# Optimization experiments

Hardware: AMD Instinct MI355X
Metric: run time of the kernel (lower is better)

## Reference

```python
import jax, jax.numpy as jnp
import numpy as np

# physics constants (match init_kwargs)
DT = 1.0 / 60.0
G_ACC = 9.81
RHO = 1.225
CD = 0.47
NU = 0.001
B, N, GRID = 512, 64, 16


def _norm(x):
    return jnp.linalg.norm(x, axis=-1, keepdims=True)


def _deriv(pos, vel, rot, omega, mass, inertia, contacts, fluid_v,
           Fext, tau, log_A, log_k, log_b, conv_w):
    g_vec = jnp.array([0.0, 0.0, -G_ACC], dtype=pos.dtype)
    Fg = mass[..., None] * g_vec                                  # [B,N,3]
    A = jax.nn.softplus(log_A).reshape(1, -1, 1)
    vm = jnp.maximum(_norm(vel), 1e-6)
    Fd = -0.5 * RHO * CD * A * vm * vel                           # drag
    k = jax.nn.softplus(log_k)
    b = jax.nn.softplus(log_b)
    d_ij = pos[:, None, :, :] - pos[:, :, None, :]                # [B,N,N,3] = p_j - p_i
    dist = jnp.maximum(_norm(d_ij), 1e-6)
    n_hat = d_ij / dist
    pen = jax.nn.relu(1.0 - dist[..., 0])                         # penetration depth
    dvel = vel[:, None, :, :] - vel[:, :, None, :]                # v_j - v_i
    Fc = (k * pen[..., None] * n_hat + b * dvel * contacts[..., None]).sum(axis=2)
    dv = (Fext + Fg + Fd + Fc) / mass[..., None]
    Io = inertia * omega
    domega = (tau - jnp.cross(omega, Io)) / jnp.maximum(inertia, 1e-6)
    w, x, y, z = rot[..., 0], rot[..., 1], rot[..., 2], rot[..., 3]
    ox, oy, oz = omega[..., 0], omega[..., 1], omega[..., 2]
    drot = 0.5 * jnp.stack([
        -x * ox - y * oy - z * oz,
        w * ox + y * oz - z * oy,
        w * oy - x * oz + z * ox,
        w * oz + x * oy - y * ox], axis=-1)
    P_in = (Fext * vel).sum((-1, -2))
    P_dis = -(Fd * vel).sum((-1, -2))
    dE = P_in - P_dis
    Bsz = fluid_v.shape[0]
    u = fluid_v.reshape(Bsz, GRID, GRID, GRID, 3).transpose(0, 4, 1, 2, 3)  # NCDHW
    dfluid = NU * jax.lax.conv_general_dilated(
        u, conv_w, window_strides=(1, 1, 1), padding=[(1, 1)] * 3,
        feature_group_count=3,
        dimension_numbers=('NCDHW', 'OIDHW', 'NCDHW'))
    dfluid = dfluid.transpose(0, 2, 3, 4, 1).reshape(Bsz, GRID ** 3, 3)
    return vel, dv, drot, domega, dE, dfluid


def _quat_normalize(q):
    return q / jnp.maximum(_norm(q), 1e-12)


def _apply(pos, vel, rot, omega, fluid_v, dt, dp, dv, dr, dw, dfluid):
    npos = pos + dt * dp
    nvel = vel + dt * dv
    nrot = _quat_normalize(rot + dt * dr)
    nomega = omega + dt * dw
    new_u = fluid_v + dt * dfluid
    nfluid = new_u - new_u.mean(axis=1, keepdims=True)
    return npos, nvel, nrot, nomega, nfluid


def _forward(pos, vel, rot, omega, mass, inertia, contacts, energy, fluid_v,
             Fext, tau, log_A, log_k, log_b, conv_w):
    dt = DT
    params = (mass, inertia, contacts)

    def deriv(p, v, r, o, fv):
        return _deriv(p, v, r, o, mass, inertia, contacts, fv,
                      Fext, tau, log_A, log_k, log_b, conv_w)

    k1 = deriv(pos, vel, rot, omega, fluid_v)
    s2 = _apply(pos, vel, rot, omega, fluid_v, dt / 2, k1[0], k1[1], k1[2], k1[3], k1[5])
    k2 = deriv(*s2)
    s3 = _apply(pos, vel, rot, omega, fluid_v, dt / 2, k2[0], k2[1], k2[2], k2[3], k2[5])
    k3 = deriv(*s3)
    s4 = _apply(pos, vel, rot, omega, fluid_v, dt, k3[0], k3[1], k3[2], k3[3], k3[5])
    k4 = deriv(*s4)

    def rk4c(y, a, b_, c, d):
        return y + dt / 6 * (a + 2 * b_ + 2 * c + d)

    npos = rk4c(pos, k1[0], k2[0], k3[0], k4[0])
    nvel = rk4c(vel, k1[1], k2[1], k3[1], k4[1])
    nrot = _quat_normalize(rk4c(rot, k1[2], k2[2], k3[2], k4[2]))
    nomega = rk4c(omega, k1[3], k2[3], k3[3], k4[3])
    nenergy = rk4c(energy, k1[4], k2[4], k3[4], k4[4])
    nforces = Fext + mass[..., None] * k1[1]
    raw_fluid = rk4c(fluid_v, k1[5], k2[5], k3[5], k4[5])
    nfluid = raw_fluid - raw_fluid.mean(axis=1, keepdims=True)
    Bsz = pos.shape[0]
    # flatten new state: [pos, vel, rot, omega, forces, energy, fluid_v]
    return jnp.concatenate([
        npos.reshape(Bsz, -1), nvel.reshape(Bsz, -1), nrot.reshape(Bsz, -1),
        nomega.reshape(Bsz, -1), nforces.reshape(Bsz, -1),
        nenergy[:, None], nfluid.reshape(Bsz, -1)], axis=-1)


def setup_inputs() -> dict:
    key = jax.random.key(0)
    ks = jax.random.split(key, 12)
    rot = jax.random.normal(ks[2], (B, N, 4), dtype=jnp.float32)
    rot = rot / jnp.maximum(jnp.linalg.norm(rot, axis=-1, keepdims=True), 1e-12)
    return {
        'pos': 2.0 * jax.random.normal(ks[0], (B, N, 3), dtype=jnp.float32),
        'vel': jax.random.normal(ks[1], (B, N, 3), dtype=jnp.float32),
        'rot': rot,
        'omega': jax.random.normal(ks[3], (B, N, 3), dtype=jnp.float32),
        'mass': 0.5 + jax.random.uniform(ks[4], (B, N), dtype=jnp.float32),
        'inertia': 0.05 + 0.1 * jax.random.uniform(ks[5], (B, N, 3), dtype=jnp.float32),
        'contacts': jax.random.uniform(ks[6], (B, N, N), dtype=jnp.float32),
        'energy': jnp.zeros((B,), dtype=jnp.float32),
        'fluid_v': jax.random.normal(ks[7], (B, GRID ** 3, 3), dtype=jnp.float32),
        'Fext': jax.random.normal(ks[8], (B, N, 3), dtype=jnp.float32),
        'tau': jax.random.normal(ks[9], (B, N, 3), dtype=jnp.float32),
        'log_A': jnp.zeros((N,), dtype=jnp.float32),
        'log_k': jnp.full((1,), np.log(1000.0), dtype=jnp.float32),
        'log_b': jnp.full((1,), np.log(10.0), dtype=jnp.float32),
        'conv_w': 0.1 * jax.random.normal(ks[10], (3, 1, 3, 3, 3), dtype=jnp.float32),
    }


def reference(pos, vel, rot, omega, mass, inertia, contacts, energy, fluid_v,
              Fext, tau, log_A, log_k, log_b, conv_w):
    return _forward(pos, vel, rot, omega, mass, inertia, contacts, energy,
                    fluid_v, Fext, tau, log_A, log_k, log_b, conv_w)
```

## Files before the change

kernel.cpp:

```cpp
#include <hip/hip_runtime.h>

#define DT (1.0f/60.0f)
#define G_ACC 9.81f
#define RHO 1.225f
#define CD_ 0.47f
#define NU 0.001f

__device__ __forceinline__ float softplus_f(float x) {
    return log1pf(expf(-fabsf(x))) + fmaxf(x, 0.0f);
}

#define RL(v, l) __int_as_float(__builtin_amdgcn_readlane(__float_as_int(v), (l)))
#define SLANE(x) __int_as_float(__builtin_amdgcn_readfirstlane(__float_as_int(x)))

__device__ __forceinline__ float dpp_xm(float v) {
    return __int_as_float(__builtin_amdgcn_update_dpp(0, __float_as_int(v), 0x111, 0xf, 0xf, true));
}
__device__ __forceinline__ float dpp_xp(float v) {
    return __int_as_float(__builtin_amdgcn_update_dpp(0, __float_as_int(v), 0x101, 0xf, 0xf, true));
}

__global__ __launch_bounds__(256) void fused_kernel(
    const float* __restrict__ pos, const float* __restrict__ vel,
    const float* __restrict__ rot, const float* __restrict__ omega,
    const float* __restrict__ mass, const float* __restrict__ inertia,
    const float* __restrict__ contacts, const float* __restrict__ energy,
    const float* __restrict__ fluid, const float* __restrict__ Fext,
    const float* __restrict__ tau, const float* __restrict__ log_A,
    const float* __restrict__ log_k, const float* __restrict__ log_b,
    const float* __restrict__ conv_w, float* __restrict__ out)
{
    __shared__ float smem[4928];
    const int t = threadIdx.x;

    if (blockIdx.x < 1536) {
        const int b  = blockIdx.x & 511;
        const int ch = blockIdx.x >> 9;
        const int x  = t & 15, y = t >> 4, wv = t >> 6;
        float* u   = smem;
        float* red = smem + 4368;
        if (t < 16) smem[4352 + t] = 0.f;

        float W[27];
        #pragma unroll
        for (int k = 0; k < 27; ++k) W[k] = NU * SLANE(conv_w[ch*27 + k]);

        const int lb = t*17;
        const float* fb = fluid + (size_t)b*12288 + 3*t + ch;
        float base[16], acc[16];
        #pragma unroll
        for (int z = 0; z < 16; ++z) {
            float v = fb[z*768];
            base[z] = v; acc[z] = 0.f; u[lb + z] = v;
        }

        const float xm = (x > 0) ? 1.f : 0.f, xp = (x < 15) ? 1.f : 0.f;
        const float mm = (y > 0) ? 1.f : 0.f, pm = (y < 15) ? 1.f : 0.f;
        float Sdz0, Sdz1, Sdz2;
        {
            float a0 = W[0]*xm + W[1] + W[2]*xp;
            float a1 = W[3]*xm + W[4] + W[5]*xp;
            float a2 = W[6]*xm + W[7] + W[8]*xp;
            Sdz0 = mm*a0 + a1 + pm*a2;
            a0 = W[ 9]*xm + W[10] + W[11]*xp;
            a1 = W[12]*xm + W[13] + W[14]*xp;
            a2 = W[15]*xm + W[16] + W[17]*xp;
            Sdz1 = mm*a0 + a1 + pm*a2;
            a0 = W[18]*xm + W[19] + W[20]*xp;
            a1 = W[21]*xm + W[22] + W[23]*xp;
            a2 = W[24]*xm + W[25] + W[26]*xp;
            Sdz2 = mm*a0 + a1 + pm*a2;
        }
        const float SzLo = Sdz1 + Sdz2, SzHi = Sdz0 + Sdz1, SzMid = Sdz0 + Sdz1 + Sdz2;
        const int cm = (y > 0)  ? lb - 272 : 4352;
        const int cp = (y < 15) ? lb + 272 : 4352;

        __syncthreads();
        float mean = 0.f;

        #define SEC(ca, dy) { \
            _Pragma("unroll") \
            for (int z = 0; z < 16; ++z) { \
                float c  = u[(ca) + z]; \
                float cl = dpp_xm(c), cr = dpp_xp(c); \
                o[z] += W[9+(dy)*3+1]*c + W[9+(dy)*3]*cl + W[9+(dy)*3+2]*cr; \
                if (z < 15) o[z+1] += W[(dy)*3+1]*c + W[(dy)*3]*cl + W[(dy)*3+2]*cr; \
                if (z > 0)  o[z-1] += W[18+(dy)*3+1]*c + W[18+(dy)*3]*cl + W[18+(dy)*3+2]*cr; \
            } }

        #pragma unroll
        for (int s = 0; s < 4; ++s) {
            float o[16];
            #pragma unroll
            for (int z = 0; z < 16; ++z) o[z] = 0.f;
            SEC(lb, 1);
            SEC(cm, 0);
            SEC(cp, 2);

            if (s < 3) {
                const float h = (s == 2) ? DT : DT*0.5f;
                const float w = (s == 0) ? 1.f : 2.f;
                float ps = 0.f;
                #pragma unroll
                for (int z = 0; z < 16; ++z) {
                    float Sz = (z == 0) ? SzLo : ((z == 15) ? SzHi : SzMid);
                    float k = o[z] - mean * Sz;
                    acc[z] += w * k;
                    float v = base[z] + h * k;
                    o[z] = v; ps += v;
                }
                #pragma unroll
                for (int off = 32; off > 0; off >>= 1) ps += __shfl_xor(ps, off, 64);
                __syncthreads();
                #pragma unroll
                for (int z = 0; z < 16; ++z) u[lb + z] = o[z];
                if ((t & 63) == 0) red[wv] = ps;
                __syncthreads();
                mean = (red[0] + red[1] + red[2] + red[3]) * (1.0f/4096.0f);
            } else {
                #pragma unroll
                for (int z = 0; z < 16; ++z) {
                    float Sz = (z == 0) ? SzLo : ((z == 15) ? SzHi : SzMid);
                    acc[z] += o[z] - mean * Sz;
                }
            }
        }
        #undef SEC

        float ps = 0.f;
        float o[16];
        #pragma unroll
        for (int z = 0; z < 16; ++z) { o[z] = base[z] + (DT/6.0f)*acc[z]; ps += o[z]; }
        #pragma unroll
        for (int off = 32; off > 0; off >>= 1) ps += __shfl_xor(ps, off, 64);
        __syncthreads();
        if ((t & 63) == 0) red[wv] = ps;
        __syncthreads();
        const float mn = (red[0] + red[1] + red[2] + red[3]) * (1.0f/4096.0f);

        float* ob = out + (size_t)b*13313 + 1025 + 3*t + ch;
        #pragma unroll
        for (int z = 0; z < 16; ++z) ob[z*768] = o[z] - mn;
        return;
    }

    const int b = blockIdx.x - 1536;
    const int q = t >> 6;
    const int i = t & 63;
    float* cont = smem;
    float* sF   = smem + 4160;

    {
        const float4* cg = (const float4*)(contacts + (size_t)b*4096);
        #pragma unroll
        for (int v = 0; v < 4; ++v) {
            float4 c4 = cg[v*256 + t];
            int fi = (v*256 + t) * 4;
            int r = fi >> 6, cc = fi & 63;
            float* p = cont + r*65 + cc;
            p[0] = c4.x; p[1] = c4.y; p[2] = c4.z; p[3] = c4.w;
        }
    }

    const size_t p3 = ((size_t)b*64 + i)*3;
    const size_t p4 = ((size_t)b*64 + i)*4;
    float bpx=pos[p3],   bpy=pos[p3+1],   bpz=pos[p3+2];
    float bvx=vel[p3],   bvy=vel[p3+1],   bvz=vel[p3+2];
    float brw=rot[p4],   brx=rot[p4+1],   bry=rot[p4+2],  brz=rot[p4+3];
    float box=omega[p3], boy=omega[p3+1], boz=omega[p3+2];
    float m  = mass[(size_t)b*64+i];
    float Ix=inertia[p3], Iy=inertia[p3+1], Iz=inertia[p3+2];
    float Fex=Fext[p3],   Fey=Fext[p3+1],   Fez=Fext[p3+2];
    float tx=tau[p3],     ty=tau[p3+1],     tz=tau[p3+2];
    float dragc = -0.5f * RHO * CD_ * softplus_f(log_A[i]);
    float kc = softplus_f(SLANE(log_k[0]));
    float bc = softplus_f(SLANE(log_b[0]));
    float invm = 1.0f / m;
    float iIx = 1.0f/fmaxf(Ix,1e-6f), iIy = 1.0f/fmaxf(Iy,1e-6f), iIz = 1.0f/fmaxf(Iz,1e-6f);

    float cpx=bpx, cpy=bpy, cpz=bpz;
    float cvx=bvx, cvy=bvy, cvz=bvz;
    float crw=brw, crx=brx, cry=bry, crz=brz;
    float cox=box, coy=boy, coz=boz;

    float apx=0,apy=0,apz=0, avx=0,avy=0,avz=0;
    float arw=0,arx=0,ary=0,arz=0, awx=0,awy=0,awz=0;
    float eacc=0.f;

    const int j0 = q << 4;
    float* ob = out + (size_t)b * 13313;
    __syncthreads();

    #pragma unroll
    for (int s = 0; s < 4; ++s) {
        float Fcx=0.f, Fcy=0.f, Fcz=0.f;
        #pragma unroll
        for (int jj = 0; jj < 16; ++jj) {
            const int j = j0 + jj;
            float pjx = RL(cpx, j), pjy = RL(cpy, j), pjz = RL(cpz, j);
            float vjx = RL(cvx, j), vjy = RL(cvy, j), vjz = RL(cvz, j);
            float dx = pjx - cpx, dy = pjy - cpy, dz = pjz - cpz;
            float dist = fmaxf(sqrtf(dx*dx + dy*dy + dz*dz), 1e-6f);
            float pen  = fmaxf(1.0f - dist, 0.0f);
            float coef = kc * pen * __builtin_amdgcn_rcpf(dist);
            float cbj  = bc * cont[i*65 + j];
            Fcx += coef*dx + cbj*(vjx - cvx);
            Fcy += coef*dy + cbj*(vjy - cvy);
            Fcz += coef*dz + cbj*(vjz - cvz);
        }
        sF[q*192 + i*3+0] = Fcx;
        sF[q*192 + i*3+1] = Fcy;
        sF[q*192 + i*3+2] = Fcz;
        __syncthreads();
        Fcx = sF[i*3+0] + sF[192+i*3+0] + sF[384+i*3+0] + sF[576+i*3+0];
        Fcy = sF[i*3+1] + sF[192+i*3+1] + sF[384+i*3+1] + sF[576+i*3+1];
        Fcz = sF[i*3+2] + sF[192+i*3+2] + sF[384+i*3+2] + sF[576+i*3+2];

        float vm = fmaxf(sqrtf(cvx*cvx+cvy*cvy+cvz*cvz), 1e-6f);
        float dc = dragc * vm;
        float Fdx = dc*cvx, Fdy = dc*cvy, Fdz = dc*cvz;

        float dvx = (Fex + Fdx + Fcx) * invm;
        float dvy = (Fey + Fdy + Fcy) * invm;
        float dvz = (Fez - m*G_ACC + Fdz + Fcz) * invm;

        if (s == 0 && q == 0) {
            ob[832 + i*3+0] = Fex + m*dvx;
            ob[832 + i*3+1] = Fey + m*dvy;
            ob[832 + i*3+2] = Fez + m*dvz;
        }

        float dqw = 0.5f*(-crx*cox - cry*coy - crz*coz);
        float dqx = 0.5f*( crw*cox + cry*coz - crz*coy);
        float dqy = 0.5f*( crw*coy - crx*coz + crz*cox);
        float dqz = 0.5f*( crw*coz + crx*coy - cry*cox);

        float Iox = Ix*cox, Ioy = Iy*coy, Ioz = Iz*coz;
        float dwx = (tx - (coy*Ioz - coz*Ioy)) * iIx;
        float dwy = (ty - (coz*Iox - cox*Ioz)) * iIy;
        float dwz = (tz - (cox*Ioy - coy*Iox)) * iIz;

        float ei = (Fex+Fdx)*cvx + (Fey+Fdy)*cvy + (Fez+Fdz)*cvz;
        #pragma unroll
        for (int off = 32; off > 0; off >>= 1) ei += __shfl_xor(ei, off, 64);

        const float w = (s == 0 || s == 3) ? 1.f : 2.f;
        eacc += w * ei;
        apx += w*cvx; apy += w*cvy; apz += w*cvz;
        avx += w*dvx; avy += w*dvy; avz += w*dvz;
        arw += w*dqw; arx += w*dqx; ary += w*dqy; arz += w*dqz;
        awx += w*dwx; awy += w*dwy; awz += w*dwz;

        if (s < 3) {
            const float h = (s == 2) ? DT : DT*0.5f;
            float npx = bpx + h*cvx, npy = bpy + h*cvy, npz = bpz + h*cvz;
            cvx = bvx + h*dvx; cvy = bvy + h*dvy; cvz = bvz + h*dvz;
            cpx = npx; cpy = npy; cpz = npz;
            float qw = brw + h*dqw, qx = brx + h*dqx, qy = bry + h*dqy, qz = brz + h*dqz;
            float iqn = 1.0f / fmaxf(sqrtf(qw*qw+qx*qx+qy*qy+qz*qz), 1e-12f);
            crw = qw*iqn; crx = qx*iqn; cry = qy*iqn; crz = qz*iqn;
            cox = box + h*dwx; coy = boy + h*dwy; coz = boz + h*dwz;
            __syncthreads();
        }
    }

    if (q == 0) {
        const float s6 = DT / 6.0f;
        ob[      i*3+0] = bpx + s6*apx;  ob[      i*3+1] = bpy + s6*apy;  ob[      i*3+2] = bpz + s6*apz;
        ob[192 + i*3+0] = bvx + s6*avx;  ob[192 + i*3+1] = bvy + s6*avy;  ob[192 + i*3+2] = bvz + s6*avz;
        {
            float qw=brw+s6*arw, qx=brx+s6*arx, qy=bry+s6*ary, qz=brz+s6*arz;
            float iq = 1.0f / fmaxf(sqrtf(qw*qw+qx*qx+qy*qy+qz*qz), 1e-12f);
            ob[384 + i*4+0]=qw*iq; ob[384 + i*4+1]=qx*iq; ob[384 + i*4+2]=qy*iq; ob[384 + i*4+3]=qz*iq;
        }
        ob[640 + i*3+0] = box + s6*awx;  ob[640 + i*3+1] = boy + s6*awy;  ob[640 + i*3+2] = boz + s6*awz;
        if (i == 0) ob[1024] = energy[b] + s6*eacc;
    }
}

extern "C" void kernel_launch(void* const* d_in, const int* in_sizes, int n_in,
                              void* d_out, int out_size, void* d_ws, size_t ws_size,
                              hipStream_t stream) {
    const float* pos      = (const float*)d_in[0];
    const float* vel      = (const float*)d_in[1];
    const float* rot      = (const float*)d_in[2];
    const float* omega    = (const float*)d_in[3];
    const float* mass     = (const float*)d_in[4];
    const float* inertia  = (const float*)d_in[5];
    const float* contacts = (const float*)d_in[6];
    const float* energy   = (const float*)d_in[7];
    const float* fluid_v  = (const float*)d_in[8];
    const float* Fext     = (const float*)d_in[9];
    const float* tau      = (const float*)d_in[10];
    const float* log_A    = (const float*)d_in[11];
    const float* log_k    = (const float*)d_in[12];
    const float* log_b    = (const float*)d_in[13];
    const float* conv_w   = (const float*)d_in[14];
    float* out = (float*)d_out;

    fused_kernel<<<dim3(2048), dim3(256), 0, stream>>>(
        pos, vel, rot, omega, mass, inertia, contacts, energy, fluid_v,
        Fext, tau, log_A, log_k, log_b, conv_w, out);
}
```

Measured before the change: 187.1 us.

## Split fluid stencil z-range across two thread halves with double-buffered LDS

Blocks grow from 256 to 512 threads. In the fluid blocks each column's 16 z-planes are split between two halves of 8, with a 10-value halo load per neighbour row. Ping-pong shared buffers remove one barrier per RK stage, and per-stage reduction slots prevent overwrite races. The particle blocks now split the j-loop over 8 wave groups instead of 4. This adds parallelism and cuts per-thread register arrays, at the cost of extra halo loads, larger LDS use and more partial sums to reduce.

```diff
diff --git a/kernel.cpp b/kernel.cpp
--- a/kernel.cpp
+++ b/kernel.cpp
@@ -20,7 +20,7 @@
     return __int_as_float(__builtin_amdgcn_update_dpp(0, __float_as_int(v), 0x101, 0xf, 0xf, true));
 }
 
-__global__ __launch_bounds__(256) void fused_kernel(
+__global__ __launch_bounds__(512) void fused_kernel(
     const float* __restrict__ pos, const float* __restrict__ vel,
     const float* __restrict__ rot, const float* __restrict__ omega,
     const float* __restrict__ mass, const float* __restrict__ inertia,
@@ -30,28 +30,32 @@
     const float* __restrict__ log_k, const float* __restrict__ log_b,
     const float* __restrict__ conv_w, float* __restrict__ out)
 {
-    __shared__ float smem[4928];
+    __shared__ float smem[8772];
     const int t = threadIdx.x;
 
     if (blockIdx.x < 1536) {
-        const int b  = blockIdx.x & 511;
-        const int ch = blockIdx.x >> 9;
-        const int x  = t & 15, y = t >> 4, wv = t >> 6;
-        float* u   = smem;
-        float* red = smem + 4368;
-        if (t < 16) smem[4352 + t] = 0.f;
+        const int b   = blockIdx.x & 511;
+        const int ch  = blockIdx.x >> 9;
+        const int col = t & 255;
+        const int h   = t >> 8;
+        const int x   = col & 15, y = col >> 4, wv = t >> 6;
+        const int h8  = h << 3;
+        float* red = smem + 8740;
 
         float W[27];
         #pragma unroll
         for (int k = 0; k < 27; ++k) W[k] = NU * SLANE(conv_w[ch*27 + k]);
 
-        const int lb = t*17;
-        const float* fb = fluid + (size_t)b*12288 + 3*t + ch;
-        float base[16], acc[16];
-        #pragma unroll
-        for (int z = 0; z < 16; ++z) {
-            float v = fb[z*768];
-            base[z] = v; acc[z] = 0.f; u[lb + z] = v;
+        const int lb = col*17;
+        if (t < 18) { smem[4352 + t] = 0.f; smem[4370 + 4352 + t] = 0.f; }
+
+        const float* fb = fluid + (size_t)b*12288 + 3*col + ch;
+        float base[8], acc[8];
+        #pragma unroll
+        for (int zz = 0; zz < 8; ++zz) {
+            float v = fb[(h8 + zz)*768];
+            base[zz] = v; acc[zz] = 0.f;
+            smem[lb + h8 + zz] = v;
         }
 
         const float xm = (x > 0) ? 1.f : 0.f, xp = (x < 15) ? 1.f : 0.f;
@@ -71,76 +75,95 @@
             a2 = W[24]*xm + W[25] + W[26]*xp;
             Sdz2 = mm*a0 + a1 + pm*a2;
         }
-        const float SzLo = Sdz1 + Sdz2, SzHi = Sdz0 + Sdz1, SzMid = Sdz0 + Sdz1 + Sdz2;
-        const int cm = (y > 0)  ? lb - 272 : 4352;
-        const int cp = (y < 15) ? lb + 272 : 4352;
+        const float SzLo = Sdz1 + Sdz2;
+        const float SzHi = Sdz0 + Sdz1;
+        const float SzMid = Sdz0 + Sdz1 + Sdz2;
+
+        const int ownR = lb + h8 - 1;
+        const int cmR  = (y > 0)  ? (lb - 272 + h8 - 1) : 4353;
+        const int cpR  = (y < 15) ? (lb + 272 + h8 - 1) : 4353;
 
         __syncthreads();
         float mean = 0.f;
 
-        #define SEC(ca, dy) { \
-            _Pragma("unroll") \
-            for (int z = 0; z < 16; ++z) { \
-                float c  = u[(ca) + z]; \
-                float cl = dpp_xm(c), cr = dpp_xp(c); \
-                o[z] += W[9+(dy)*3+1]*c + W[9+(dy)*3]*cl + W[9+(dy)*3+2]*cr; \
-                if (z < 15) o[z+1] += W[(dy)*3+1]*c + W[(dy)*3]*cl + W[(dy)*3+2]*cr; \
-                if (z > 0)  o[z-1] += W[18+(dy)*3+1]*c + W[18+(dy)*3]*cl + W[18+(dy)*3+2]*cr; \
+        #define LOADC(cidx) { \
+            const float* Up = smem + rb + (cidx); \
+            if (h == 0) { c[0] = 0.f; \
+                _Pragma("unroll") for (int k = 1; k < 10; ++k) c[k] = Up[k]; } \
+            else { \
+                _Pragma("unroll") for (int k = 0; k < 9; ++k) c[k] = Up[k]; \
+                c[9] = 0.f; } }
+
+        #define SCAT(wy) { \
+            _Pragma("unroll") for (int k = 0; k < 10; ++k) { \
+                float cc = c[k], cl = dpp_xm(cc), cr = dpp_xp(cc); \
+                if (k < 8) \
+                    o[k]   += W[(wy)*3+0]*cl + W[(wy)*3+1]*cc + W[(wy)*3+2]*cr; \
+                if (k >= 1 && k <= 8) \
+                    o[k-1] += W[9+(wy)*3+0]*cl + W[9+(wy)*3+1]*cc + W[9+(wy)*3+2]*cr; \
+                if (k >= 2) \
+                    o[k-2] += W[18+(wy)*3+0]*cl + W[18+(wy)*3+1]*cc + W[18+(wy)*3+2]*cr; \
             } }
 
         #pragma unroll
         for (int s = 0; s < 4; ++s) {
-            float o[16];
+            const int rb = (s & 1) * 4370;
+            const int wb = 4370 - rb;
+            float o[8];
             #pragma unroll
-            for (int z = 0; z < 16; ++z) o[z] = 0.f;
-            SEC(lb, 1);
-            SEC(cm, 0);
-            SEC(cp, 2);
+            for (int zz = 0; zz < 8; ++zz) o[zz] = 0.f;
+            {
+                float c[10];
+                LOADC(ownR); SCAT(1);
+                LOADC(cmR);  SCAT(0);
+                LOADC(cpR);  SCAT(2);
+            }
 
             if (s < 3) {
-                const float h = (s == 2) ? DT : DT*0.5f;
+                const float hstep = (s == 2) ? DT : DT*0.5f;
                 const float w = (s == 0) ? 1.f : 2.f;
                 float ps = 0.f;
                 #pragma unroll
-                for (int z = 0; z < 16; ++z) {
-                    float Sz = (z == 0) ? SzLo : ((z == 15) ? SzHi : SzMid);
-                    float k = o[z] - mean * Sz;
-                    acc[z] += w * k;
-                    float v = base[z] + h * k;
-                    o[z] = v; ps += v;
+                for (int zz = 0; zz < 8; ++zz) {
+                    float Sz = (h == 0 && zz == 0) ? SzLo
+                             : ((h == 1 && zz == 7) ? SzHi : SzMid);
+                    float k = o[zz] - mean * Sz;
+                    acc[zz] += w * k;
+                    float v = base[zz] + hstep * k;
+                    smem[wb + lb + h8 + zz] = v;
+                    ps += v;
                 }
                 #pragma unroll
                 for (int off = 32; off > 0; off >>= 1) ps += __shfl_xor(ps, off, 64);
+                if ((t & 63) == 0) red[s*8 + wv] = ps;
                 __syncthreads();
-                #pragma unroll
-                for (int z = 0; z < 16; ++z) u[lb + z] = o[z];
-                if ((t & 63) == 0) red[wv] = ps;
-                __syncthreads();
-                mean = (red[0] + red[1] + red[2] + red[3]) * (1.0f/4096.0f);
+                mean = (red[s*8+0]+red[s*8+1]+red[s*8+2]+red[s*8+3]
+                       +red[s*8+4]+red[s*8+5]+red[s*8+6]+red[s*8+7]) * (1.0f/4096.0f);
             } else {
                 #pragma unroll
-                for (int z = 0; z < 16; ++z) {
-                    float Sz = (z == 0) ? SzLo : ((z == 15) ? SzHi : SzMid);
-                    acc[z] += o[z] - mean * Sz;
+                for (int zz = 0; zz < 8; ++zz) {
+                    float Sz = (h == 0 && zz == 0) ? SzLo
+                             : ((h == 1 && zz == 7) ? SzHi : SzMid);
+                    acc[zz] += o[zz] - mean * Sz;
                 }
             }
         }
-        #undef SEC
-
-        float ps = 0.f;
-        float o[16];
-        #pragma unroll
-        for (int z = 0; z < 16; ++z) { o[z] = base[z] + (DT/6.0f)*acc[z]; ps += o[z]; }
+        #undef LOADC
+        #undef SCAT
+
+        float raw[8], ps = 0.f;
+        #pragma unroll
+        for (int zz = 0; zz < 8; ++zz) { raw[zz] = base[zz] + (DT/6.0f)*acc[zz]; ps += raw[zz]; }
         #pragma unroll
         for (int off = 32; off > 0; off >>= 1) ps += __shfl_xor(ps, off, 64);
+        if ((t & 63) == 0) red[24 + wv] = ps;
         __syncthreads();
-        if ((t & 63) == 0) red[wv] = ps;
-        __syncthreads();
-        const float mn = (red[0] + red[1] + red[2] + red[3]) * (1.0f/4096.0f);
-
-        float* ob = out + (size_t)b*13313 + 1025 + 3*t + ch;
-        #pragma unroll
-        for (int z = 0; z < 16; ++z) ob[z*768] = o[z] - mn;
+        const float mn = (red[24]+red[25]+red[26]+red[27]
+                         +red[28]+red[29]+red[30]+red[31]) * (1.0f/4096.0f);
+
+        float* ob = out + (size_t)b*13313 + 1025 + 3*col + ch;
+        #pragma unroll
+        for (int zz = 0; zz < 8; ++zz) ob[(h8 + zz)*768] = raw[zz] - mn;
         return;
     }
 
@@ -153,9 +176,9 @@
     {
         const float4* cg = (const float4*)(contacts + (size_t)b*4096);
         #pragma unroll
-        for (int v = 0; v < 4; ++v) {
-            float4 c4 = cg[v*256 + t];
-            int fi = (v*256 + t) * 4;
+        for (int v = 0; v < 2; ++v) {
+            float4 c4 = cg[v*512 + t];
+            int fi = (v*512 + t) * 4;
             int r = fi >> 6, cc = fi & 63;
             float* p = cont + r*65 + cc;
             p[0] = c4.x; p[1] = c4.y; p[2] = c4.z; p[3] = c4.w;
@@ -187,7 +210,7 @@
     float arw=0,arx=0,ary=0,arz=0, awx=0,awy=0,awz=0;
     float eacc=0.f;
 
-    const int j0 = q << 4;
+    const int j0 = q << 3;
     float* ob = out + (size_t)b * 13313;
     __syncthreads();
 
@@ -195,7 +218,7 @@
     for (int s = 0; s < 4; ++s) {
         float Fcx=0.f, Fcy=0.f, Fcz=0.f;
         #pragma unroll
-        for (int jj = 0; jj < 16; ++jj) {
+        for (int jj = 0; jj < 8; ++jj) {
             const int j = j0 + jj;
             float pjx = RL(cpx, j), pjy = RL(cpy, j), pjz = RL(cpz, j);
             float vjx = RL(cvx, j), vjy = RL(cvy, j), vjz = RL(cvz, j);
@@ -212,9 +235,13 @@
         sF[q*192 + i*3+1] = Fcy;
         sF[q*192 + i*3+2] = Fcz;
         __syncthreads();
-        Fcx = sF[i*3+0] + sF[192+i*3+0] + sF[384+i*3+0] + sF[576+i*3+0];
-        Fcy = sF[i*3+1] + sF[192+i*3+1] + sF[384+i*3+1] + sF[576+i*3+1];
-        Fcz = sF[i*3+2] + sF[192+i*3+2] + sF[384+i*3+2] + sF[576+i*3+2];
+        Fcx = 0.f; Fcy = 0.f; Fcz = 0.f;
+        #pragma unroll
+        for (int qq = 0; qq < 8; ++qq) {
+            Fcx += sF[qq*192 + i*3+0];
+            Fcy += sF[qq*192 + i*3+1];
+            Fcz += sF[qq*192 + i*3+2];
+        }
 
         float vm = fmaxf(sqrtf(cvx*cvx+cvy*cvy+cvz*cvz), 1e-6f);
         float dc = dragc * vm;
@@ -298,7 +325,7 @@
     const float* conv_w   = (const float*)d_in[14];
     float* out = (float*)d_out;
 
-    fused_kernel<<<dim3(2048), dim3(256), 0, stream>>>(
+    fused_kernel<<<dim3(2048), dim3(512), 0, stream>>>(
         pos, vel, rot, omega, mass, inertia, contacts, energy, fluid_v,
         Fext, tau, log_A, log_k, log_b, conv_w, out);
 }
```

Measured after the change: 182.3 us. -2.6%, faster.
